# Optimization experiments

Measured on AMD Instinct MI355X. Metric: run time of the kernel, lower is better.

## Reference

```python
import jax, jax.numpy as jnp
import numpy as np

D_MODEL = 512
N_HEADS = 8
D_K = D_MODEL // N_HEADS
MAX_LEN = 512  # max_seq_len; rel table has 2*MAX_LEN-1 rows


def setup_inputs() -> dict:
    key = jax.random.key(0)
    ks = jax.random.split(key, 7)
    B, S = 8, 512
    s = 1.0 / np.sqrt(D_MODEL)
    return {
        "x": jax.random.normal(ks[0], (B, S, D_MODEL), jnp.float32),
        "Wq": jax.random.normal(ks[1], (D_MODEL, D_MODEL), jnp.float32) * s,
        "bq": jnp.zeros((D_MODEL,), jnp.float32),
        "Wk": jax.random.normal(ks[2], (D_MODEL, D_MODEL), jnp.float32) * s,
        "bk": jnp.zeros((D_MODEL,), jnp.float32),
        "Wv": jax.random.normal(ks[3], (D_MODEL, D_MODEL), jnp.float32) * s,
        "bv": jnp.zeros((D_MODEL,), jnp.float32),
        "Wo": jax.random.normal(ks[4], (D_MODEL, D_MODEL), jnp.float32) * s,
        "bo": jnp.zeros((D_MODEL,), jnp.float32),
        "rel_embed": jax.random.normal(ks[5], (2 * MAX_LEN - 1, D_MODEL), jnp.float32) * 0.02,
    }


def reference(x, Wq, bq, Wk, bk, Wv, bv, Wo, bo, rel_embed):
    B, S, _ = x.shape
    scale = np.sqrt(D_K).astype(np.float32)

    def split_heads(t):  # (B,S,D) -> (B,H,S,dk)
        return t.reshape(B, S, N_HEADS, D_K).transpose(0, 2, 1, 3)

    q = split_heads(x @ Wq.T + bq)
    k = split_heads(x @ Wk.T + bk)
    v = split_heads(x @ Wv.T + bv)

    scores = jnp.einsum('bhqd,bhkd->bhqk', q, k) / scale

    # relative position bias: idx[q_pos, k_pos] = k_pos - q_pos + MAX_LEN - 1
    pos = jnp.arange(S)
    rel_idx = pos[None, :] - pos[:, None] + (MAX_LEN - 1)  # (S,S)
    rel_bias = rel_embed[rel_idx].reshape(S, S, N_HEADS, D_K)  # (S,S,H,dk)
    scores = scores + jnp.einsum('bhqd,qkhd->bhqk', q, rel_bias)

    attn = jax.nn.softmax(scores, axis=-1)
    out = jnp.einsum('bhqk,bhkd->bhqd', attn, v)  # (B,H,S,dk)
    out = out.transpose(0, 2, 1, 3).reshape(B, S, D_MODEL)
    return out @ Wo.T + bo
```

## Files before the change

kernel.cpp:

```cpp
#include <hip/hip_runtime.h>
#include <math.h>

#define B_  8
#define S_  512
#define D_  512
#define H_  8
#define DK_ 64

typedef __attribute__((ext_vector_type(8))) short short8;
typedef __attribute__((ext_vector_type(4))) float f32x4;

#define MFMA_BF16(a, b, c) __builtin_amdgcn_mfma_f32_16x16x32_bf16(a, b, c, 0, 0, 0)

__device__ __forceinline__ unsigned bf16_rne(float x) {
    unsigned u = __float_as_uint(x);
    return (u + 0x7FFFu + ((u >> 16) & 1u)) >> 16;
}
__device__ __forceinline__ float bf16f(unsigned h) { return __uint_as_float(h << 16); }

__device__ __forceinline__ void glds16(const ushort* g, ushort* l) {
    __builtin_amdgcn_global_load_lds(
        (const __attribute__((address_space(1))) unsigned int*)g,
        (__attribute__((address_space(3))) unsigned int*)l,
        16, 0, 0);
}

__global__ __launch_bounds__(256)
void conv_pl(const float* __restrict__ x,
             const float* __restrict__ wq, const float* __restrict__ wk,
             const float* __restrict__ wv, const float* __restrict__ wo,
             ushort* __restrict__ Xh, ushort* __restrict__ Xl,
             ushort* __restrict__ Wqh, ushort* __restrict__ Wql,
             ushort* __restrict__ Wkh, ushort* __restrict__ Wkl,
             ushort* __restrict__ Wvh, ushort* __restrict__ Wvl,
             ushort* __restrict__ Woh, ushort* __restrict__ Wol) {
    const int bid = blockIdx.x;
    const float* src; ushort* dh; ushort* dl; int i4;
    if (bid < 2048) {
        src = x; dh = Xh; dl = Xl; i4 = bid * 256 + threadIdx.x;
    } else {
        const int r = bid - 2048;
        const int wsel = r >> 8;
        src = (wsel == 0) ? wq : (wsel == 1) ? wk : (wsel == 2) ? wv : wo;
        dh  = (wsel == 0) ? Wqh : (wsel == 1) ? Wkh : (wsel == 2) ? Wvh : Woh;
        dl  = (wsel == 0) ? Wql : (wsel == 1) ? Wkl : (wsel == 2) ? Wvl : Wol;
        i4 = (r & 255) * 256 + threadIdx.x;
    }
    const float4 v = ((const float4*)src)[i4];
    unsigned h[4], l[4];
    const float* vp = &v.x;
    #pragma unroll
    for (int j = 0; j < 4; ++j) { h[j] = bf16_rne(vp[j]); l[j] = bf16_rne(vp[j] - bf16f(h[j])); }
    ((uint2*)dh)[i4] = make_uint2(h[0] | (h[1] << 16), h[2] | (h[3] << 16));
    ((uint2*)dl)[i4] = make_uint2(l[0] | (l[1] << 16), l[2] | (l[3] << 16));
}

__global__ __launch_bounds__(256)
void conv_rel(const float* __restrict__ rel, ushort* __restrict__ Rg) {
    const int idx = blockIdx.x * 256 + threadIdx.x;
    const int d2 = idx & 31;
    const int rr = (idx >> 5) % 1152;
    const int h  = idx / (1152 * 32);
    unsigned v0 = 0, v1 = 0;
    if (rr >= 64 && rr < 64 + 1023) {
        const float* s = &rel[(size_t)(rr - 64) * 512 + h * 64 + d2 * 2];
        v0 = bf16_rne(s[0]); v1 = bf16_rne(s[1]);
    }
    *(uint*)&Rg[((size_t)h * 1152 + rr) * 64 + d2 * 2] = v0 | (v1 << 16);
}

template<int XB, int OM>
__global__ __launch_bounds__(256, 2)
void gemm_mfma(const ushort* __restrict__ Xhp, const ushort* __restrict__ Xlp,
               const ushort* __restrict__ Yh0, const ushort* __restrict__ Yl0,
               const ushort* __restrict__ Yh1, const ushort* __restrict__ Yl1,
               const float* __restrict__ bias0, const float* __restrict__ bias1,
               float* __restrict__ outF,
               ushort* __restrict__ oh0, ushort* __restrict__ ol0,
               ushort* __restrict__ oh1, ushort* __restrict__ ol1) {
    __shared__ ushort Xs[2][2][64 * 64];
    __shared__ ushort Ys[2][2][64 * 64];

    const int z = blockIdx.z;
    const ushort* Yhp = z ? Yh1 : Yh0;
    const ushort* Ylp = z ? Yl1 : Yl0;
    const float*  bias = z ? bias1 : bias0;
    ushort* ohp = z ? oh1 : oh0;
    ushort* olp = z ? ol1 : ol0;

    const int tid = threadIdx.x;
    const int w = tid >> 6, lane = tid & 63;
    const int g = lane >> 4, c = lane & 15;
    const int rloc = lane >> 3, cc8 = lane & 7;
    const int cp = cc8 ^ rloc;
    const int r0 = blockIdx.y * 64;
    const int c0 = blockIdx.x * 64;

    const f32x4 fz = {0.f, 0.f, 0.f, 0.f};
    f32x4 acc[2][2] = {{fz, fz}, {fz, fz}};

    auto stage = [&](int kt, int buf) {
        const int k0 = kt * 64;
        const ushort* gb; ushort* lb; size_t rstr;
        if (w < 2) {
            const ushort* Xp = (w == 1) ? Xlp : Xhp;
            if (XB == 0) { gb = Xp + (size_t)r0 * 512 + k0; rstr = 512; }
            else {
                const int b = r0 >> 9, s0 = r0 & 511, h = k0 >> 6;
                gb = Xp + (((size_t)(b * 8 + h)) * 512 + s0) * 64; rstr = 64;
            }
            lb = &Xs[buf][w][0];
        } else {
            gb = ((w == 2) ? Yhp : Ylp) + (size_t)c0 * 512 + k0; rstr = 512;
            lb = &Ys[buf][w - 2][0];
        }
        #pragma unroll
        for (int j = 0; j < 8; ++j)
            glds16(gb + (size_t)(j * 8 + rloc) * rstr + cp * 8, lb + j * 512);
    };

    auto compute = [&](int buf) {
        #pragma unroll
        for (int ks = 0; ks < 2; ++ks) {
            short8 axh[2], axl[2], byh[2], byl[2];
            const int wm = (w >> 1) * 32, wn = (w & 1) * 32;
            #pragma unroll
            for (int t = 0; t < 2; ++t) {
                int row = wm + t * 16 + c;
                int off = row * 64 + (((ks * 4 + g) ^ (row & 7)) * 8);
                axh[t] = *(const short8*)&Xs[buf][0][off];
                axl[t] = *(const short8*)&Xs[buf][1][off];
                row = wn + t * 16 + c;
                off = row * 64 + (((ks * 4 + g) ^ (row & 7)) * 8);
                byh[t] = *(const short8*)&Ys[buf][0][off];
                byl[t] = *(const short8*)&Ys[buf][1][off];
            }
            #pragma unroll
            for (int tm = 0; tm < 2; ++tm)
                #pragma unroll
                for (int tn = 0; tn < 2; ++tn) {
                    acc[tm][tn] = MFMA_BF16(axh[tm], byh[tn], acc[tm][tn]);
                    acc[tm][tn] = MFMA_BF16(axl[tm], byh[tn], acc[tm][tn]);
                    acc[tm][tn] = MFMA_BF16(axh[tm], byl[tn], acc[tm][tn]);
                }
        }
    };

    stage(0, 0);
    __syncthreads();
    for (int kt = 0; kt < 8; ++kt) {
        if (kt < 7) stage(kt + 1, (kt + 1) & 1);
        compute(kt & 1);
        __syncthreads();
    }

    const int wm = (w >> 1) * 32, wn = (w & 1) * 32;
    if (OM == 0) {
        #pragma unroll
        for (int tn = 0; tn < 2; ++tn) {
            const int gc = c0 + wn + tn * 16 + c;
            const float bv = bias[gc];
            #pragma unroll
            for (int tm = 0; tm < 2; ++tm)
                #pragma unroll
                for (int i = 0; i < 4; ++i) {
                    const int gr = r0 + wm + tm * 16 + g * 4 + i;
                    outF[(size_t)gr * 512 + gc] = acc[tm][tn][i] + bv;
                }
        }
    } else if (OM == 2) {
        #pragma unroll
        for (int tn = 0; tn < 2; ++tn) {
            const int gc = c0 + wn + tn * 16 + c;
            const int h = gc >> 6, dk = gc & 63;
            const float bv = bias[gc];
            #pragma unroll
            for (int tm = 0; tm < 2; ++tm)
                #pragma unroll
                for (int i = 0; i < 4; ++i) {
                    const int gr = r0 + wm + tm * 16 + g * 4 + i;
                    const int b = gr >> 9, s = gr & 511;
                    const float v = acc[tm][tn][i] + bv;
                    const unsigned hb = bf16_rne(v);
                    const size_t a = (((size_t)(b * 8 + h)) * 512 + s) * 64 + dk;
                    ohp[a] = (ushort)hb;
                    olp[a] = (ushort)bf16_rne(v - bf16f(hb));
                }
        }
    } else {
        #pragma unroll
        for (int tm = 0; tm < 2; ++tm)
            #pragma unroll
            for (int i = 0; i < 4; ++i) {
                const int gr = r0 + wm + tm * 16 + g * 4 + i;
                const int h = gr >> 6, dk = gr & 63;
                const float bv = bias[gr];
                #pragma unroll
                for (int tn = 0; tn < 2; ++tn) {
                    const int gc = c0 + wn + tn * 16 + c;
                    const int b = gc >> 9, s = gc & 511;
                    const float v = acc[tm][tn][i] + bv;
                    const size_t a = (((size_t)(b * 8 + h)) * 64 + dk) * 512 + s;
                    ohp[a] = (ushort)bf16_rne(v);
                }
            }
    }
}

__global__ __launch_bounds__(256, 4)
void attn_mfma(const ushort* __restrict__ Qhp, const ushort* __restrict__ Qlp,
               const ushort* __restrict__ Khp, const ushort* __restrict__ Klp,
               const ushort* __restrict__ Vhp, const ushort* __restrict__ Rg,
               float* __restrict__ Op0, float* __restrict__ Op1,
               float2* __restrict__ Ml0, float2* __restrict__ Ml1) {
    __shared__ ushort Ksm[2][64 * 64];
    __shared__ ushort Vsm[64 * 64];
    __shared__ float  Psm[4][16 * 64];

    const int tid  = threadIdx.x;
    const int w    = tid >> 6;
    const int lane = tid & 63;
    const int g    = lane >> 4;
    const int c    = lane & 15;
    const int rloc = lane >> 3, cc8 = lane & 7;
    const int cp   = cc8 ^ rloc;
    const int bh   = blockIdx.y;
    const int h    = bh & 7;
    const int z    = blockIdx.z;
    const int qw   = blockIdx.x * 64 + w * 16;

    float* __restrict__ Op = z ? Op1 : Op0;
    float2* __restrict__ Ml = z ? Ml1 : Ml0;

    short8 qfh[2], qfl[2];
    #pragma unroll
    for (int ks = 0; ks < 2; ++ks) {
        const size_t qi = ((size_t)bh * 512 + qw + c) * 64 + ks * 32 + g * 8;
        qfh[ks] = *(const short8*)&Qhp[qi];
        qfl[ks] = *(const short8*)&Qlp[qi];
    }

    const f32x4 fz = {0.f, 0.f, 0.f, 0.f};
    f32x4 o[4] = {fz, fz, fz, fz};
    float mreg[4], lreg[4];
    #pragma unroll
    for (int i = 0; i < 4; ++i) { mreg[i] = -INFINITY; lreg[i] = 0.f; }

    const ushort* KhB = Khp + (size_t)bh * 512 * 64;
    const ushort* KlB = Klp + (size_t)bh * 512 * 64;
    const ushort* VhB = Vhp + (size_t)bh * 64 * 512;

    for (int kt = z * 4; kt < z * 4 + 4; ++kt) {
        const int k0 = kt * 64;
        __syncthreads();
        if (w < 2) {
            const ushort* gb = (w == 0 ? KhB : KlB) + (size_t)k0 * 64;
            ushort* lb = &Ksm[w][0];
            #pragma unroll
            for (int j = 0; j < 8; ++j)
                glds16(gb + (size_t)(j * 8 + rloc) * 64 + cp * 8, lb + j * 512);
        } else {
            const ushort* gb = VhB + k0 + (size_t)(w - 2) * 32 * 512;
            ushort* lb = &Vsm[(w - 2) * 32 * 64];
            #pragma unroll
            for (int j = 0; j < 4; ++j)
                glds16(gb + (size_t)(j * 8 + rloc) * 512 + cp * 8, lb + j * 512);
        }
        __syncthreads();

        f32x4 u[5];
        #pragma unroll
        for (int ut = 0; ut < 5; ++ut) u[ut] = fz;
        const int rrow0 = k0 - qw + 559 + c;
        #pragma unroll
        for (int ks = 0; ks < 2; ++ks)
            #pragma unroll
            for (int ut = 0; ut < 5; ++ut) {
                const short8 rf = *(const short8*)
                    &Rg[((size_t)h * 1152 + rrow0 + ut * 16) * 64 + ks * 32 + g * 8];
                u[ut] = MFMA_BF16(qfh[ks], rf, u[ut]);
            }

        f32x4 s[4];
        #pragma unroll
        for (int tc = 0; tc < 4; ++tc) s[tc] = fz;
        #pragma unroll
        for (int ks = 0; ks < 2; ++ks)
            #pragma unroll
            for (int tc = 0; tc < 4; ++tc) {
                const int row = tc * 16 + c;
                const int chv = ((ks * 4 + g) ^ (row & 7)) * 8;
                const short8 kh8 = *(const short8*)&Ksm[0][row * 64 + chv];
                const short8 kl8 = *(const short8*)&Ksm[1][row * 64 + chv];
                s[tc] = MFMA_BF16(qfh[ks], kh8, s[tc]);
                s[tc] = MFMA_BF16(qfl[ks], kh8, s[tc]);
                s[tc] = MFMA_BF16(qfh[ks], kl8, s[tc]);
            }

        #pragma unroll
        for (int i = 0; i < 4; ++i) {
            const int r = g * 4 + i;
            const int srcl = (g << 4) | ((c - r) & 15);
            float sv[4];
            #pragma unroll
            for (int tc = 0; tc < 4; ++tc) {
                const float va = __shfl(u[tc + 1][i], srcl);
                const float vb = __shfl(u[tc][i], srcl);
                sv[tc] = s[tc][i] * 0.125f + ((c >= r) ? va : vb);
            }
            float tm = fmaxf(fmaxf(sv[0], sv[1]), fmaxf(sv[2], sv[3]));
            tm = fmaxf(tm, __shfl_xor(tm, 1));
            tm = fmaxf(tm, __shfl_xor(tm, 2));
            tm = fmaxf(tm, __shfl_xor(tm, 4));
            tm = fmaxf(tm, __shfl_xor(tm, 8));
            const float mold = mreg[i];
            const float mn = fmaxf(mold, tm);
            const float corr = __expf(mold - mn);
            mreg[i] = mn;
            float lacc = lreg[i] * corr;
            #pragma unroll
            for (int dt = 0; dt < 4; ++dt) o[dt][i] *= corr;
            #pragma unroll
            for (int tc = 0; tc < 4; ++tc) {
                const float p = __expf(sv[tc] - mn);
                lacc += p;
                const int col = tc * 16 + c;
                Psm[w][r * 64 + (((col >> 2) ^ r) << 2) + (col & 3)] = p;
            }
            lreg[i] = lacc;
        }
        asm volatile("s_waitcnt lgkmcnt(0)" ::: "memory");

        #pragma unroll
        for (int ks = 0; ks < 2; ++ks) {
            const int pc0 = ks * 8 + g * 2;
            const f32x4 pa = *(const f32x4*)&Psm[w][c * 64 + ((pc0 ^ c) << 2)];
            const f32x4 pb = *(const f32x4*)&Psm[w][c * 64 + (((pc0 + 1) ^ c) << 2)];
            short8 aph, apl;
            #pragma unroll
            for (int j = 0; j < 8; ++j) {
                const float pj = (j < 4) ? pa[j] : pb[j - 4];
                const unsigned hbits = bf16_rne(pj);
                aph[j] = (short)hbits;
                apl[j] = (short)bf16_rne(pj - bf16f(hbits));
            }
            #pragma unroll
            for (int dt = 0; dt < 4; ++dt) {
                const int row = dt * 16 + c;
                const int chv = ((ks * 4 + g) ^ (row & 7)) * 8;
                const short8 vh8 = *(const short8*)&Vsm[row * 64 + chv];
                o[dt] = MFMA_BF16(aph, vh8, o[dt]);
                o[dt] = MFMA_BF16(apl, vh8, o[dt]);
            }
        }
    }

    #pragma unroll
    for (int i = 0; i < 4; ++i) {
        float ls = lreg[i];
        ls += __shfl_xor(ls, 1);
        ls += __shfl_xor(ls, 2);
        ls += __shfl_xor(ls, 4);
        ls += __shfl_xor(ls, 8);
        const int r = g * 4 + i;
        const size_t rowi = (size_t)bh * 512 + qw + r;
        if (c == 0) Ml[rowi] = make_float2(mreg[i], ls);
        #pragma unroll
        for (int dt = 0; dt < 4; ++dt)
            Op[rowi * 64 + dt * 16 + c] = o[dt][i];
    }
}

__global__ __launch_bounds__(256)
void attn_combine(const float* __restrict__ Op0, const float* __restrict__ Op1,
                  const float2* __restrict__ Ml0, const float2* __restrict__ Ml1,
                  ushort* __restrict__ Oh, ushort* __restrict__ Ol) {
    const int tid = threadIdx.x;
    const int row = blockIdx.x * 64 + (tid >> 2);
    const int d0 = (tid & 3) * 16;
    const float2 a = Ml0[row], b = Ml1[row];
    const float m = fmaxf(a.x, b.x);
    float w0 = __expf(a.x - m), w1 = __expf(b.x - m);
    const float inv = 1.0f / (a.y * w0 + b.y * w1);
    w0 *= inv; w1 *= inv;
    const size_t base = (size_t)row * 64 + d0;
    #pragma unroll
    for (int j = 0; j < 4; ++j) {
        const float4 v0 = *(const float4*)&Op0[base + j * 4];
        const float4 v1 = *(const float4*)&Op1[base + j * 4];
        float vv[4] = {v0.x * w0 + v1.x * w1, v0.y * w0 + v1.y * w1,
                       v0.z * w0 + v1.z * w1, v0.w * w0 + v1.w * w1};
        unsigned hb[4], lb4[4];
        #pragma unroll
        for (int q = 0; q < 4; ++q) {
            hb[q] = bf16_rne(vv[q]);
            lb4[q] = bf16_rne(vv[q] - bf16f(hb[q]));
        }
        *(uint2*)&Oh[base + j * 4] = make_uint2(hb[0] | (hb[1] << 16), hb[2] | (hb[3] << 16));
        *(uint2*)&Ol[base + j * 4] = make_uint2(lb4[0] | (lb4[1] << 16), lb4[2] | (lb4[3] << 16));
    }
}

extern "C" void kernel_launch(void* const* d_in, const int* in_sizes, int n_in,
                              void* d_out, int out_size, void* d_ws, size_t ws_size,
                              hipStream_t stream) {
    const float* x   = (const float*)d_in[0];
    const float* Wq  = (const float*)d_in[1];
    const float* bq  = (const float*)d_in[2];
    const float* Wk  = (const float*)d_in[3];
    const float* bk  = (const float*)d_in[4];
    const float* Wv  = (const float*)d_in[5];
    const float* bv  = (const float*)d_in[6];
    const float* Wo  = (const float*)d_in[7];
    const float* bo  = (const float*)d_in[8];
    const float* rel = (const float*)d_in[9];
    float* out = (float*)d_out;

    const size_t NP = (size_t)B_ * H_ * S_ * DK_;
    const size_t WP = (size_t)D_ * D_;
    ushort* Xh  = (ushort*)d_ws;
    ushort* Xl  = Xh + NP;
    ushort* Wqh = Xl + NP;
    ushort* Wql = Wqh + WP;
    ushort* Wkh = Wql + WP;
    ushort* Wkl = Wkh + WP;
    ushort* Wvh = Wkl + WP;
    ushort* Wvl = Wvh + WP;
    ushort* Woh = Wvl + WP;
    ushort* Wol = Woh + WP;
    ushort* Qh  = Wol + WP;
    ushort* Ql  = Qh + NP;
    ushort* Kh  = Ql + NP;
    ushort* Kl  = Kh + NP;
    ushort* Vh  = Kl + NP;
    ushort* Rg  = Vh + NP;
    float*  Op1 = (float*)(Rg + 589824);
    float2* Ml0 = (float2*)(Op1 + NP);
    float2* Ml1 = Ml0 + 32768;
    float*  Op0 = (float*)d_ws;

    conv_pl<<<3072, 256, 0, stream>>>(x, Wq, Wk, Wv, Wo,
                                      Xh, Xl, Wqh, Wql, Wkh, Wkl, Wvh, Wvl, Woh, Wol);
    conv_rel<<<1152, 256, 0, stream>>>(rel, Rg);

    gemm_mfma<0, 2><<<dim3(8, 64, 2), 256, 0, stream>>>(
        Xh, Xl, Wqh, Wql, Wkh, Wkl, bq, bk, nullptr, Qh, Ql, Kh, Kl);
    gemm_mfma<0, 3><<<dim3(64, 8, 1), 256, 0, stream>>>(
        Wvh, Wvl, Xh, Xl, nullptr, nullptr, bv, nullptr, nullptr, Vh, nullptr, nullptr, nullptr);

    attn_mfma<<<dim3(8, 64, 2), 256, 0, stream>>>(
        Qh, Ql, Kh, Kl, Vh, Rg, Op0, Op1, Ml0, Ml1);

    attn_combine<<<512, 256, 0, stream>>>(Op0, Op1, Ml0, Ml1, Kh, Kl);

    gemm_mfma<1, 0><<<dim3(8, 64, 1), 256, 0, stream>>>(
        Kh, Kl, Woh, Wol, nullptr, nullptr, bo, nullptr, out, nullptr, nullptr, nullptr, nullptr);
}
```

Measured before the change: 107.9 us.

## Compute transposed scores in attention, drop P lo-split and shuffle-based rel-bias

Attention now computes S^T (keys on rows) so each lane owns one query column, reducing the softmax max/sum to two cross-group shuffles instead of four per row. The relative-bias skew goes through a small bf16 LDS buffer instead of per-element shuffles, and K rows are loaded in a permuted order so the P fragment feeds the PV MFMA straight from registers, skipping the Psm round-trip. The 1/8 scale is folded into K in the projection GEMM. P is now single bf16 (no lo-part MFMA), which halves PV MFMA work but lowers precision. The output is written transposed, so the combine kernel stages it through LDS. Occupancy hint drops from 4 to 3.

```diff
diff --git a/kernel.cpp b/kernel.cpp
--- a/kernel.cpp
+++ b/kernel.cpp
@@ -75,6 +75,7 @@
                const ushort* __restrict__ Yh0, const ushort* __restrict__ Yl0,
                const ushort* __restrict__ Yh1, const ushort* __restrict__ Yl1,
                const float* __restrict__ bias0, const float* __restrict__ bias1,
+               float scale0, float scale1,
                float* __restrict__ outF,
                ushort* __restrict__ oh0, ushort* __restrict__ ol0,
                ushort* __restrict__ oh1, ushort* __restrict__ ol1) {
@@ -85,6 +86,7 @@
     const ushort* Yhp = z ? Yh1 : Yh0;
     const ushort* Ylp = z ? Yl1 : Yl0;
     const float*  bias = z ? bias1 : bias0;
+    const float   scale = z ? scale1 : scale0;
     ushort* ohp = z ? oh1 : oh0;
     ushort* olp = z ? ol1 : ol0;
 
@@ -180,7 +182,7 @@
                 for (int i = 0; i < 4; ++i) {
                     const int gr = r0 + wm + tm * 16 + g * 4 + i;
                     const int b = gr >> 9, s = gr & 511;
-                    const float v = acc[tm][tn][i] + bv;
+                    const float v = (acc[tm][tn][i] + bv) * scale;
                     const unsigned hb = bf16_rne(v);
                     const size_t a = (((size_t)(b * 8 + h)) * 512 + s) * 64 + dk;
                     ohp[a] = (ushort)hb;
@@ -207,7 +209,7 @@
     }
 }
 
-__global__ __launch_bounds__(256, 4)
+__global__ __launch_bounds__(256, 3)
 void attn_mfma(const ushort* __restrict__ Qhp, const ushort* __restrict__ Qlp,
                const ushort* __restrict__ Khp, const ushort* __restrict__ Klp,
                const ushort* __restrict__ Vhp, const ushort* __restrict__ Rg,
@@ -215,7 +217,7 @@
                float2* __restrict__ Ml0, float2* __restrict__ Ml1) {
     __shared__ ushort Ksm[2][64 * 64];
     __shared__ ushort Vsm[64 * 64];
-    __shared__ float  Psm[4][16 * 64];
+    __shared__ ushort Usm[4][16 * 86];
 
     const int tid  = threadIdx.x;
     const int w    = tid >> 6;
@@ -223,7 +225,6 @@
     const int g    = lane >> 4;
     const int c    = lane & 15;
     const int rloc = lane >> 3, cc8 = lane & 7;
-    const int cp   = cc8 ^ rloc;
     const int bh   = blockIdx.y;
     const int h    = bh & 7;
     const int z    = blockIdx.z;
@@ -242,9 +243,7 @@
 
     const f32x4 fz = {0.f, 0.f, 0.f, 0.f};
     f32x4 o[4] = {fz, fz, fz, fz};
-    float mreg[4], lreg[4];
-    #pragma unroll
-    for (int i = 0; i < 4; ++i) { mreg[i] = -INFINITY; lreg[i] = 0.f; }
+    float m = -INFINITY, l = 0.f;
 
     const ushort* KhB = Khp + (size_t)bh * 512 * 64;
     const ushort* KlB = Klp + (size_t)bh * 512 * 64;
@@ -254,24 +253,31 @@
         const int k0 = kt * 64;
         __syncthreads();
         if (w < 2) {
-            const ushort* gb = (w == 0 ? KhB : KlB) + (size_t)k0 * 64;
+            const ushort* gb = (w == 0) ? KhB : KlB;
             ushort* lb = &Ksm[w][0];
             #pragma unroll
-            for (int j = 0; j < 8; ++j)
-                glds16(gb + (size_t)(j * 8 + rloc) * 64 + cp * 8, lb + j * 512);
+            for (int j = 0; j < 8; ++j) {
+                const int row = j * 8 + rloc;
+                const int tcq = row >> 4, cq = row & 15;
+                const int key = ((tcq & 1) << 5) + ((cq >> 2) << 3)
+                              + ((tcq >> 1) << 2) + (cq & 3);
+                glds16(gb + (size_t)(k0 + key) * 64 + (cc8 ^ rloc) * 8,
+                       lb + j * 512);
+            }
         } else {
             const ushort* gb = VhB + k0 + (size_t)(w - 2) * 32 * 512;
             ushort* lb = &Vsm[(w - 2) * 32 * 64];
             #pragma unroll
             for (int j = 0; j < 4; ++j)
-                glds16(gb + (size_t)(j * 8 + rloc) * 512 + cp * 8, lb + j * 512);
+                glds16(gb + (size_t)(j * 8 + rloc) * 512 + (cc8 ^ rloc) * 8,
+                       lb + j * 512);
         }
         __syncthreads();
 
         f32x4 u[5];
         #pragma unroll
         for (int ut = 0; ut < 5; ++ut) u[ut] = fz;
-        const int rrow0 = k0 - qw + 559 + c;
+        const int rrow0 = k0 - qw + 560 + c;
         #pragma unroll
         for (int ks = 0; ks < 2; ++ks)
             #pragma unroll
@@ -280,10 +286,15 @@
                     &Rg[((size_t)h * 1152 + rrow0 + ut * 16) * 64 + ks * 32 + g * 8];
                 u[ut] = MFMA_BF16(qfh[ks], rf, u[ut]);
             }
-
-        f32x4 s[4];
-        #pragma unroll
-        for (int tc = 0; tc < 4; ++tc) s[tc] = fz;
+        #pragma unroll
+        for (int ut = 0; ut < 5; ++ut)
+            #pragma unroll
+            for (int i = 0; i < 4; ++i)
+                Usm[w][(g * 4 + i) * 86 + c + ut * 16] = (ushort)bf16_rne(u[ut][i]);
+
+        f32x4 st[4];
+        #pragma unroll
+        for (int tc = 0; tc < 4; ++tc) st[tc] = fz;
         #pragma unroll
         for (int ks = 0; ks < 2; ++ks)
             #pragma unroll
@@ -292,112 +303,116 @@
                 const int chv = ((ks * 4 + g) ^ (row & 7)) * 8;
                 const short8 kh8 = *(const short8*)&Ksm[0][row * 64 + chv];
                 const short8 kl8 = *(const short8*)&Ksm[1][row * 64 + chv];
-                s[tc] = MFMA_BF16(qfh[ks], kh8, s[tc]);
-                s[tc] = MFMA_BF16(qfl[ks], kh8, s[tc]);
-                s[tc] = MFMA_BF16(qfh[ks], kl8, s[tc]);
-            }
-
-        #pragma unroll
-        for (int i = 0; i < 4; ++i) {
-            const int r = g * 4 + i;
-            const int srcl = (g << 4) | ((c - r) & 15);
-            float sv[4];
-            #pragma unroll
-            for (int tc = 0; tc < 4; ++tc) {
-                const float va = __shfl(u[tc + 1][i], srcl);
-                const float vb = __shfl(u[tc][i], srcl);
-                sv[tc] = s[tc][i] * 0.125f + ((c >= r) ? va : vb);
-            }
-            float tm = fmaxf(fmaxf(sv[0], sv[1]), fmaxf(sv[2], sv[3]));
-            tm = fmaxf(tm, __shfl_xor(tm, 1));
-            tm = fmaxf(tm, __shfl_xor(tm, 2));
-            tm = fmaxf(tm, __shfl_xor(tm, 4));
-            tm = fmaxf(tm, __shfl_xor(tm, 8));
-            const float mold = mreg[i];
-            const float mn = fmaxf(mold, tm);
-            const float corr = __expf(mold - mn);
-            mreg[i] = mn;
-            float lacc = lreg[i] * corr;
-            #pragma unroll
-            for (int dt = 0; dt < 4; ++dt) o[dt][i] *= corr;
-            #pragma unroll
-            for (int tc = 0; tc < 4; ++tc) {
-                const float p = __expf(sv[tc] - mn);
-                lacc += p;
-                const int col = tc * 16 + c;
-                Psm[w][r * 64 + (((col >> 2) ^ r) << 2) + (col & 3)] = p;
-            }
-            lreg[i] = lacc;
-        }
+                st[tc] = MFMA_BF16(kh8, qfh[ks], st[tc]);
+                st[tc] = MFMA_BF16(kh8, qfl[ks], st[tc]);
+                st[tc] = MFMA_BF16(kl8, qfh[ks], st[tc]);
+            }
+
         asm volatile("s_waitcnt lgkmcnt(0)" ::: "memory");
 
         #pragma unroll
+        for (int tc = 0; tc < 4; ++tc)
+            #pragma unroll
+            for (int i = 0; i < 4; ++i) {
+                const int key = ((tc & 1) << 5) + 8 * g + ((tc >> 1) << 2) + i;
+                st[tc][i] += bf16f(Usm[w][c * 85 + key + 15]);
+            }
+
+        float tm = fmaxf(fmaxf(st[0][0], st[0][1]), fmaxf(st[0][2], st[0][3]));
+        #pragma unroll
+        for (int tc = 1; tc < 4; ++tc) {
+            const float t2 = fmaxf(fmaxf(st[tc][0], st[tc][1]),
+                                   fmaxf(st[tc][2], st[tc][3]));
+            tm = fmaxf(tm, t2);
+        }
+        tm = fmaxf(tm, __shfl_xor(tm, 16));
+        tm = fmaxf(tm, __shfl_xor(tm, 32));
+        const float mn = fmaxf(m, tm);
+        const float corr = __expf(m - mn);
+        m = mn;
+        l *= corr;
+        #pragma unroll
+        for (int dt = 0; dt < 4; ++dt) o[dt] *= corr;
+
+        uint pk[4][2];
+        #pragma unroll
+        for (int tc = 0; tc < 4; ++tc) {
+            const float p0 = __expf(st[tc][0] - mn);
+            const float p1 = __expf(st[tc][1] - mn);
+            const float p2 = __expf(st[tc][2] - mn);
+            const float p3 = __expf(st[tc][3] - mn);
+            l += (p0 + p1) + (p2 + p3);
+            pk[tc][0] = bf16_rne(p0) | (bf16_rne(p1) << 16);
+            pk[tc][1] = bf16_rne(p2) | (bf16_rne(p3) << 16);
+        }
+
+        #pragma unroll
         for (int ks = 0; ks < 2; ++ks) {
-            const int pc0 = ks * 8 + g * 2;
-            const f32x4 pa = *(const f32x4*)&Psm[w][c * 64 + ((pc0 ^ c) << 2)];
-            const f32x4 pb = *(const f32x4*)&Psm[w][c * 64 + (((pc0 + 1) ^ c) << 2)];
-            short8 aph, apl;
-            #pragma unroll
-            for (int j = 0; j < 8; ++j) {
-                const float pj = (j < 4) ? pa[j] : pb[j - 4];
-                const unsigned hbits = bf16_rne(pj);
-                aph[j] = (short)hbits;
-                apl[j] = (short)bf16_rne(pj - bf16f(hbits));
-            }
+            union { uint u4[4]; short8 s8; } pb;
+            pb.u4[0] = pk[ks][0];
+            pb.u4[1] = pk[ks][1];
+            pb.u4[2] = pk[ks + 2][0];
+            pb.u4[3] = pk[ks + 2][1];
             #pragma unroll
             for (int dt = 0; dt < 4; ++dt) {
                 const int row = dt * 16 + c;
                 const int chv = ((ks * 4 + g) ^ (row & 7)) * 8;
                 const short8 vh8 = *(const short8*)&Vsm[row * 64 + chv];
-                o[dt] = MFMA_BF16(aph, vh8, o[dt]);
-                o[dt] = MFMA_BF16(apl, vh8, o[dt]);
-            }
-        }
-    }
-
+                o[dt] = MFMA_BF16(vh8, pb.s8, o[dt]);
+            }
+        }
+    }
+
+    float lt = l;
+    lt += __shfl_xor(lt, 16);
+    lt += __shfl_xor(lt, 32);
+    if (lane < 16) Ml[(size_t)bh * 512 + qw + c] = make_float2(m, lt);
     #pragma unroll
-    for (int i = 0; i < 4; ++i) {
-        float ls = lreg[i];
-        ls += __shfl_xor(ls, 1);
-        ls += __shfl_xor(ls, 2);
-        ls += __shfl_xor(ls, 4);
-        ls += __shfl_xor(ls, 8);
-        const int r = g * 4 + i;
-        const size_t rowi = (size_t)bh * 512 + qw + r;
-        if (c == 0) Ml[rowi] = make_float2(mreg[i], ls);
-        #pragma unroll
-        for (int dt = 0; dt < 4; ++dt)
-            Op[rowi * 64 + dt * 16 + c] = o[dt][i];
-    }
+    for (int dt = 0; dt < 4; ++dt)
+        #pragma unroll
+        for (int i = 0; i < 4; ++i)
+            Op[((size_t)bh * 64 + dt * 16 + g * 4 + i) * 512 + qw + c] = o[dt][i];
 }
 
 __global__ __launch_bounds__(256)
 void attn_combine(const float* __restrict__ Op0, const float* __restrict__ Op1,
                   const float2* __restrict__ Ml0, const float2* __restrict__ Ml1,
                   ushort* __restrict__ Oh, ushort* __restrict__ Ol) {
-    const int tid = threadIdx.x;
-    const int row = blockIdx.x * 64 + (tid >> 2);
-    const int d0 = (tid & 3) * 16;
-    const float2 a = Ml0[row], b = Ml1[row];
-    const float m = fmaxf(a.x, b.x);
-    float w0 = __expf(a.x - m), w1 = __expf(b.x - m);
+    __shared__ float L0[64][67];
+    __shared__ float L1[64][67];
+    const int t = threadIdx.x;
+    const int bh = blockIdx.y;
+    const int s0 = blockIdx.x * 64;
+    #pragma unroll
+    for (int j = 0; j < 4; ++j) {
+        const int d = (t >> 4) + j * 16;
+        const int c4 = (t & 15) * 4;
+        const size_t ga = ((size_t)bh * 64 + d) * 512 + s0 + c4;
+        *(float4*)&L0[d][c4] = *(const float4*)&Op0[ga];
+        *(float4*)&L1[d][c4] = *(const float4*)&Op1[ga];
+    }
+    __syncthreads();
+    const int sl = t >> 2;
+    const int d0 = (t & 3) * 16;
+    const float2 a = Ml0[(size_t)bh * 512 + s0 + sl];
+    const float2 b = Ml1[(size_t)bh * 512 + s0 + sl];
+    const float mm = fmaxf(a.x, b.x);
+    float w0 = __expf(a.x - mm), w1 = __expf(b.x - mm);
     const float inv = 1.0f / (a.y * w0 + b.y * w1);
     w0 *= inv; w1 *= inv;
-    const size_t base = (size_t)row * 64 + d0;
+    const size_t ob = ((size_t)bh * 512 + s0 + sl) * 64 + d0;
     #pragma unroll
-    for (int j = 0; j < 4; ++j) {
-        const float4 v0 = *(const float4*)&Op0[base + j * 4];
-        const float4 v1 = *(const float4*)&Op1[base + j * 4];
-        float vv[4] = {v0.x * w0 + v1.x * w1, v0.y * w0 + v1.y * w1,
-                       v0.z * w0 + v1.z * w1, v0.w * w0 + v1.w * w1};
+    for (int q = 0; q < 4; ++q) {
         unsigned hb[4], lb4[4];
         #pragma unroll
-        for (int q = 0; q < 4; ++q) {
-            hb[q] = bf16_rne(vv[q]);
-            lb4[q] = bf16_rne(vv[q] - bf16f(hb[q]));
-        }
-        *(uint2*)&Oh[base + j * 4] = make_uint2(hb[0] | (hb[1] << 16), hb[2] | (hb[3] << 16));
-        *(uint2*)&Ol[base + j * 4] = make_uint2(lb4[0] | (lb4[1] << 16), lb4[2] | (lb4[3] << 16));
+        for (int e = 0; e < 4; ++e) {
+            const int dd = q * 4 + e;
+            const float v = L0[d0 + dd][sl] * w0 + L1[d0 + dd][sl] * w1;
+            hb[e] = bf16_rne(v);
+            lb4[e] = bf16_rne(v - bf16f(hb[e]));
+        }
+        *(uint2*)&Oh[ob + q * 4] = make_uint2(hb[0] | (hb[1] << 16), hb[2] | (hb[3] << 16));
+        *(uint2*)&Ol[ob + q * 4] = make_uint2(lb4[0] | (lb4[1] << 16), lb4[2] | (lb4[3] << 16));
     }
 }
 
@@ -444,15 +459,18 @@
     conv_rel<<<1152, 256, 0, stream>>>(rel, Rg);
 
     gemm_mfma<0, 2><<<dim3(8, 64, 2), 256, 0, stream>>>(
-        Xh, Xl, Wqh, Wql, Wkh, Wkl, bq, bk, nullptr, Qh, Ql, Kh, Kl);
+        Xh, Xl, Wqh, Wql, Wkh, Wkl, bq, bk, 1.0f, 0.125f,
+        nullptr, Qh, Ql, Kh, Kl);
     gemm_mfma<0, 3><<<dim3(64, 8, 1), 256, 0, stream>>>(
-        Wvh, Wvl, Xh, Xl, nullptr, nullptr, bv, nullptr, nullptr, Vh, nullptr, nullptr, nullptr);
+        Wvh, Wvl, Xh, Xl, nullptr, nullptr, bv, nullptr, 1.0f, 1.0f,
+        nullptr, Vh, nullptr, nullptr, nullptr);
 
     attn_mfma<<<dim3(8, 64, 2), 256, 0, stream>>>(
         Qh, Ql, Kh, Kl, Vh, Rg, Op0, Op1, Ml0, Ml1);
 
-    attn_combine<<<512, 256, 0, stream>>>(Op0, Op1, Ml0, Ml1, Kh, Kl);
+    attn_combine<<<dim3(8, 64), 256, 0, stream>>>(Op0, Op1, Ml0, Ml1, Kh, Kl);
 
     gemm_mfma<1, 0><<<dim3(8, 64, 1), 256, 0, stream>>>(
-        Kh, Kl, Woh, Wol, nullptr, nullptr, bo, nullptr, out, nullptr, nullptr, nullptr, nullptr);
-}
+        Kh, Kl, Woh, Wol, nullptr, nullptr, bo, nullptr, 1.0f, 1.0f,
+        out, nullptr, nullptr, nullptr, nullptr);
+}
```

Result: faster. 102.4 us (-5.1%).
